# Kernel optimization log

Hardware: AMD Instinct MI355X
Metric: run time of the kernel (lower is better)

## Reference

```python
import jax, jax.numpy as jnp
import numpy as np

N, A, C = 2048, 256, 100   # batch, feat_dim, num_classes
LAT = A // 2               # latent_dim = feat_dim // 2
BN_EPS = 1e-5


def setup_inputs() -> dict:
    key = jax.random.key(0)
    ks = jax.random.split(key, 8)
    s = jax.random.normal(ks[0], (N, A), dtype=jnp.float32)
    y = jax.random.randint(ks[1], (N,), 0, C)
    ratio = jnp.float32(0.5)
    W1 = jax.random.normal(ks[2], (LAT, A), dtype=jnp.float32) / np.sqrt(A)
    b1 = jnp.zeros((LAT,), jnp.float32)
    gamma = jnp.ones((LAT,), jnp.float32)
    beta = jnp.zeros((LAT,), jnp.float32)
    W2 = jax.random.normal(ks[3], (A, LAT), dtype=jnp.float32) / np.sqrt(LAT)
    b2 = jnp.zeros((A,), jnp.float32)
    Wfc = jax.random.normal(ks[4], (C, A), dtype=jnp.float32) / np.sqrt(A)
    bfc = jnp.zeros((C,), jnp.float32)
    # per-class covariance table [C, A, A], symmetric PSD like a real EstimatorCV state
    M = jax.random.normal(ks[5], (C, A, A), dtype=jnp.float32)
    cov = jnp.einsum('cab,cdb->cad', M, M) / A
    return {"s": s, "y": y, "ratio": ratio, "W1": W1, "b1": b1,
            "gamma": gamma, "beta": beta, "W2": W2, "b2": b2,
            "Wfc": Wfc, "bfc": bfc, "cov": cov}


def reference(s, y, ratio, W1, b1, gamma, beta, W2, b2, Wfc, bfc, cov):
    # pred: Linear -> BatchNorm1d (train-mode batch stats) -> ReLU -> Linear -> ReLU
    h = s @ W1.T + b1                                   # [N, LAT]
    mu = jnp.mean(h, axis=0)
    var = jnp.var(h, axis=0)                            # biased, as torch BN
    h = (h - mu) / jnp.sqrt(var + BN_EPS) * gamma + beta
    h = jax.nn.relu(h)
    f = jax.nn.relu(h @ W2.T + b2)                      # [N, A]
    z = f @ Wfc.T + bfc                                 # [N, C]

    # correct_z: diag of (W_i - W_y) cov[y] (W_i - W_y)^T, computed without the
    # wasted off-diagonal bmm of the original
    cov_sg = jax.lax.stop_gradient(cov)                 # cov is detached in source
    Wy = Wfc[y]                                         # [N, A]
    diff = Wfc[None, :, :] - Wy[:, None, :]             # [N, C, A]
    CVy = cov_sg[y]                                     # [N, A, A]
    tmp = jnp.einsum('nca,nab->ncb', diff, CVy)         # [N, C, A]
    sigma2 = jnp.sum(tmp * diff, axis=-1)               # [N, C] = diag of quad form
    return z + ratio * 0.5 * sigma2
```

## Files before the change

kernel.cpp:

```cpp
#include <hip/hip_runtime.h>
#include <hip/hip_bf16.h>

#define Nn  2048
#define Aa  256
#define Cc  100
#define LAT 128
#define BN_EPS 1e-5f

#define OFF_HB   0
#define OFF_SUMS (OFF_HB + Nn*LAT/2)
#define OFF_SP   (OFF_SUMS + 128*256)
#define OFF_W2B  (OFF_SP + 4*Cc*Cc)
#define OFF_WFB  (OFF_W2B + Aa*LAT/2)

typedef __attribute__((ext_vector_type(8))) short bf16x8;
typedef __attribute__((ext_vector_type(4))) float f32x4;

__device__ __forceinline__ short f2bf(float f) {
    return (short)__bfloat16_as_ushort(__float2bfloat16(f));
}
__device__ __forceinline__ float bf2f(short h) {
    return __uint_as_float(((unsigned)(unsigned short)h) << 16);
}

#define DPITCH 264

__global__ __launch_bounds__(256) void kA(
    const float* __restrict__ s, const float* __restrict__ W1,
    const float* __restrict__ b1, const float* __restrict__ Wfc,
    const float* __restrict__ W2, const float* __restrict__ cov,
    short* __restrict__ hB, float* __restrict__ sums, float* __restrict__ Spart,
    short* __restrict__ W2b, short* __restrict__ Wfcb)
{
    __shared__ __align__(16) char smem[112 * DPITCH * 2 + 4 * 112 * 4];
    const int bid = blockIdx.x;
    const int t = threadIdx.x;
    const int w = t >> 6, l = t & 63, il = l & 15, q = l >> 4;

    if (bid < 400) {
        short* Dlds = (short*)smem;
        float (*red)[112] = (float(*)[112])(smem + 112 * DPITCH * 2);
        const int k  = bid >> 2;
        const int nq = bid & 3;
        const float* covk = cov + (size_t)k * (Aa * Aa);

        {
            const int c4 = t & 63;
            float4 wk = *(const float4*)&Wfc[(size_t)k * Aa + c4 * 4];
#pragma unroll
            for (int j = 0; j < 28; j++) {
                int row = (t >> 6) + j * 4;
                short4 o;
                if (row < Cc) {
                    float4 v = *(const float4*)&Wfc[(size_t)row * Aa + c4 * 4];
                    o.x = f2bf(v.x - wk.x); o.y = f2bf(v.y - wk.y);
                    o.z = f2bf(v.z - wk.z); o.w = f2bf(v.w - wk.w);
                } else {
                    o.x = 0; o.y = 0; o.z = 0; o.w = 0;
                }
                *(short4*)&Dlds[row * DPITCH + c4 * 4] = o;
            }
        }
        __syncthreads();

        const int bbase = nq * 64 + w * 16;

        f32x4 acc[7];
#pragma unroll
        for (int m = 0; m < 7; m++) acc[m] = (f32x4){0.f,0.f,0.f,0.f};

        const float* brow = covk + (size_t)(bbase + il) * Aa;

#pragma unroll
        for (int sgk = 0; sgk < 8; sgk++) {
            const int a0 = sgk * 32 + q * 8;
            float4 u0 = *(const float4*)&brow[a0];
            float4 u1 = *(const float4*)&brow[a0 + 4];
            bf16x8 bm;
            bm[0]=f2bf(u0.x); bm[1]=f2bf(u0.y); bm[2]=f2bf(u0.z); bm[3]=f2bf(u0.w);
            bm[4]=f2bf(u1.x); bm[5]=f2bf(u1.y); bm[6]=f2bf(u1.z); bm[7]=f2bf(u1.w);
#pragma unroll
            for (int m = 0; m < 7; m++) {
                bf16x8 am = *(bf16x8*)&Dlds[(m * 16 + il) * DPITCH + a0];
                acc[m] = __builtin_amdgcn_mfma_f32_16x16x32_bf16(am, bm, acc[m], 0, 0, 0);
            }
        }

#pragma unroll
        for (int m = 0; m < 7; m++) {
            const int bcol = bbase + il;
            float sacc[4];
#pragma unroll
            for (int r = 0; r < 4; r++) {
                int crow = m * 16 + q * 4 + r;
                sacc[r] = bf2f(Dlds[crow * DPITCH + bcol]) * acc[m][r];
            }
#pragma unroll
            for (int r = 0; r < 4; r++) {
                float v = sacc[r];
                v += __shfl_xor(v, 1);
                v += __shfl_xor(v, 2);
                v += __shfl_xor(v, 4);
                v += __shfl_xor(v, 8);
                if (il == 0) red[w][m * 16 + q * 4 + r] = v;
            }
        }
        __syncthreads();
        if (t < Cc)
            Spart[nq * (Cc * Cc) + k * Cc + t] =
                red[0][t] + red[1][t] + red[2][t] + red[3][t];
    } else if (bid < 528) {
        const int bid2 = bid - 400;
        const int row0 = bid2 * 16;
        const int colw = w * 32;

        f32x4 acc[2];
        acc[0] = (f32x4){0.f,0.f,0.f,0.f};
        acc[1] = (f32x4){0.f,0.f,0.f,0.f};

        const float* arow = s  + (size_t)(row0 + il) * Aa;
        const float* bp0  = W1 + (size_t)(colw + il) * Aa;
        const float* bp1  = W1 + (size_t)(colw + 16 + il) * Aa;

#pragma unroll
        for (int ks = 0; ks < 8; ks++) {
            const int k0 = ks * 32 + q * 8;
            float4 u0 = *(const float4*)&arow[k0];
            float4 u1 = *(const float4*)&arow[k0 + 4];
            bf16x8 am;
            am[0]=f2bf(u0.x); am[1]=f2bf(u0.y); am[2]=f2bf(u0.z); am[3]=f2bf(u0.w);
            am[4]=f2bf(u1.x); am[5]=f2bf(u1.y); am[6]=f2bf(u1.z); am[7]=f2bf(u1.w);
            float4 v0 = *(const float4*)&bp0[k0];
            float4 v1 = *(const float4*)&bp0[k0 + 4];
            bf16x8 bm0;
            bm0[0]=f2bf(v0.x); bm0[1]=f2bf(v0.y); bm0[2]=f2bf(v0.z); bm0[3]=f2bf(v0.w);
            bm0[4]=f2bf(v1.x); bm0[5]=f2bf(v1.y); bm0[6]=f2bf(v1.z); bm0[7]=f2bf(v1.w);
            float4 x0 = *(const float4*)&bp1[k0];
            float4 x1 = *(const float4*)&bp1[k0 + 4];
            bf16x8 bm1;
            bm1[0]=f2bf(x0.x); bm1[1]=f2bf(x0.y); bm1[2]=f2bf(x0.z); bm1[3]=f2bf(x0.w);
            bm1[4]=f2bf(x1.x); bm1[5]=f2bf(x1.y); bm1[6]=f2bf(x1.z); bm1[7]=f2bf(x1.w);
            acc[0] = __builtin_amdgcn_mfma_f32_16x16x32_bf16(am, bm0, acc[0], 0, 0, 0);
            acc[1] = __builtin_amdgcn_mfma_f32_16x16x32_bf16(am, bm1, acc[1], 0, 0, 0);
        }

#pragma unroll
        for (int n = 0; n < 2; n++) {
            const int col = colw + n * 16 + il;
            const float bias = b1[col];
            float s1 = 0.f, s2 = 0.f;
#pragma unroll
            for (int r = 0; r < 4; r++) {
                float v = acc[n][r] + bias;
                hB[(size_t)(row0 + q * 4 + r) * LAT + col] = f2bf(v);
                s1 += v; s2 += v * v;
            }
            s1 += __shfl_xor(s1, 16); s1 += __shfl_xor(s1, 32);
            s2 += __shfl_xor(s2, 16); s2 += __shfl_xor(s2, 32);
            if (q == 0) {
                sums[bid2 * 256 + col]       = s1;
                sums[bid2 * 256 + 128 + col] = s2;
            }
        }
    } else if (bid == 528) {
        for (int i = t * 4; i < Aa * LAT; i += 1024) {
            float4 v = *(const float4*)&W2[i];
            short4 o = {f2bf(v.x), f2bf(v.y), f2bf(v.z), f2bf(v.w)};
            *(short4*)&W2b[i] = o;
        }
    } else {
        for (int i = t * 4; i < 128 * Aa; i += 1024) {
            int row = i >> 8;
            short4 o = {0, 0, 0, 0};
            if (row < Cc) {
                float4 v = *(const float4*)&Wfc[i];
                o.x = f2bf(v.x); o.y = f2bf(v.y); o.z = f2bf(v.z); o.w = f2bf(v.w);
            }
            *(short4*)&Wfcb[i] = o;
        }
    }
}

#define FPITCH 264

__global__ __launch_bounds__(256) void kB(
    const short* __restrict__ hB, const float* __restrict__ sums,
    const float* __restrict__ gamma, const float* __restrict__ beta,
    const short* __restrict__ W2b, const float* __restrict__ b2,
    const short* __restrict__ Wfcb, const float* __restrict__ bfc,
    const float* __restrict__ Spart, const int* __restrict__ y,
    const float* __restrict__ ratio, float* __restrict__ out)
{
    __shared__ float scL[LAT], shL[LAT];
    __shared__ short fLDS[16 * FPITCH];
    const int t = threadIdx.x;
    const int w = t >> 6, l = t & 63, il = l & 15, q = l >> 4;
    const int row0 = blockIdx.x * 16;

    if (t < 128) {
        float a1 = 0.f, a2 = 0.f;
#pragma unroll 8
        for (int b = 0; b < 128; b++) {
            a1 += sums[b * 256 + t];
            a2 += sums[b * 256 + 128 + t];
        }
        float mu  = a1 * (1.0f / Nn);
        float var = a2 * (1.0f / Nn) - mu * mu;
        float inv = rsqrtf(var + BN_EPS);
        float sc  = gamma[t] * inv;
        scL[t] = sc;
        shL[t] = beta[t] - mu * sc;
    }
    __syncthreads();

    f32x4 acc3[4];
#pragma unroll
    for (int n = 0; n < 4; n++) acc3[n] = (f32x4){0.f,0.f,0.f,0.f};

    const short* arow = hB + (size_t)(row0 + il) * LAT;
#pragma unroll
    for (int ks = 0; ks < 4; ks++) {
        const int k0 = ks * 32 + q * 8;
        bf16x8 ha = *(const bf16x8*)&arow[k0];
        bf16x8 am;
#pragma unroll
        for (int j = 0; j < 8; j++) {
            float fv = fmaf(bf2f(ha[j]), scL[k0 + j], shL[k0 + j]);
            am[j] = f2bf(fmaxf(fv, 0.f));
        }
#pragma unroll
        for (int n = 0; n < 4; n++) {
            const int col = w * 64 + n * 16 + il;
            bf16x8 bm = *(const bf16x8*)&W2b[(size_t)col * LAT + k0];
            acc3[n] = __builtin_amdgcn_mfma_f32_16x16x32_bf16(am, bm, acc3[n], 0, 0, 0);
        }
    }
#pragma unroll
    for (int n = 0; n < 4; n++) {
        const int col = w * 64 + n * 16 + il;
        const float bias = b2[col];
#pragma unroll
        for (int r = 0; r < 4; r++) {
            float v = fmaxf(acc3[n][r] + bias, 0.f);
            fLDS[(q * 4 + r) * FPITCH + col] = f2bf(v);
        }
    }
    __syncthreads();

    f32x4 acc4[2];
    acc4[0] = (f32x4){0.f,0.f,0.f,0.f};
    acc4[1] = (f32x4){0.f,0.f,0.f,0.f};
#pragma unroll
    for (int ks = 0; ks < 8; ks++) {
        const int k0 = ks * 32 + q * 8;
        bf16x8 am = *(const bf16x8*)&fLDS[il * FPITCH + k0];
#pragma unroll
        for (int n = 0; n < 2; n++) {
            const int col = w * 32 + n * 16 + il;
            bf16x8 bm = *(const bf16x8*)&Wfcb[(size_t)col * Aa + k0];
            acc4[n] = __builtin_amdgcn_mfma_f32_16x16x32_bf16(am, bm, acc4[n], 0, 0, 0);
        }
    }

    const float coef = 0.5f * ratio[0];
    const int4 yv4 = *(const int4*)&y[row0 + q * 4];
    const int yr[4] = {yv4.x, yv4.y, yv4.z, yv4.w};

#pragma unroll
    for (int n = 0; n < 2; n++) {
        const int col = w * 32 + n * 16 + il;
        if (col < Cc) {
            const float bias = bfc[col];
#pragma unroll
            for (int r = 0; r < 4; r++) {
                const float* sp = &Spart[yr[r] * Cc + col];
                float sv = sp[0] + sp[Cc*Cc] + sp[2*Cc*Cc] + sp[3*Cc*Cc];
                out[(size_t)(row0 + q * 4 + r) * Cc + col] =
                    acc4[n][r] + bias + coef * sv;
            }
        }
    }
}

extern "C" void kernel_launch(void* const* d_in, const int* in_sizes, int n_in,
                              void* d_out, int out_size, void* d_ws, size_t ws_size,
                              hipStream_t stream)
{
    const float* s     = (const float*)d_in[0];
    const int*   y     = (const int*)  d_in[1];
    const float* ratio = (const float*)d_in[2];
    const float* W1    = (const float*)d_in[3];
    const float* b1    = (const float*)d_in[4];
    const float* gamma = (const float*)d_in[5];
    const float* beta  = (const float*)d_in[6];
    const float* W2    = (const float*)d_in[7];
    const float* b2    = (const float*)d_in[8];
    const float* Wfc   = (const float*)d_in[9];
    const float* bfc   = (const float*)d_in[10];
    const float* cov   = (const float*)d_in[11];
    float* out = (float*)d_out;
    float* ws  = (float*)d_ws;

    short* hB    = (short*)(ws + OFF_HB);
    float* sums  = ws + OFF_SUMS;
    float* Spart = ws + OFF_SP;
    short* W2b   = (short*)(ws + OFF_W2B);
    short* Wfcb  = (short*)(ws + OFF_WFB);

    hipLaunchKernelGGL(kA, dim3(530), dim3(256), 0, stream,
                       s, W1, b1, Wfc, W2, cov, hB, sums, Spart, W2b, Wfcb);
    hipLaunchKernelGGL(kB, dim3(128), dim3(256), 0, stream,
                       hB, sums, gamma, beta, W2b, b2, Wfcb, bfc, Spart, y, ratio, out);
}
```

Before: 35.24 us.

## Split sigma table blocks by class-row chunk and half of covariance columns

Each of the 400 sigma-table blocks previously covered all 112 padded class rows against a quarter of the covariance columns, so every block built the full Wfc-difference tile in LDS. Blocks now take a 64- or 48-row chunk of class rows against half of the covariance columns, with two column tiles per wave. This shrinks LDS use and the per-block diff-build work, and halves the number of partial sums the final kernel must add. In exchange each covariance row is read by two blocks instead of one, and the 48-row blocks do less work than the 64-row ones, so load is uneven.

Measured after the change: 34.80 us. About the same (-1.2%).

```diff
diff --git a/kernel.cpp b/kernel.cpp
--- a/kernel.cpp
+++ b/kernel.cpp
@@ -10,7 +10,7 @@
 #define OFF_HB   0
 #define OFF_SUMS (OFF_HB + Nn*LAT/2)
 #define OFF_SP   (OFF_SUMS + 128*256)
-#define OFF_W2B  (OFF_SP + 4*Cc*Cc)
+#define OFF_W2B  (OFF_SP + 2*Cc*Cc)
 #define OFF_WFB  (OFF_W2B + Aa*LAT/2)
 
 typedef __attribute__((ext_vector_type(8))) short bf16x8;
@@ -24,6 +24,99 @@
 }
 
 #define DPITCH 264
+
+template<int MSZ>
+__device__ __forceinline__ void ks_body(
+    const float* __restrict__ Wfc, const float* __restrict__ cov,
+    float* __restrict__ Spart, short* Dlds, float (*red)[64],
+    int k, int ch, int bh, int t, int w, int il, int q)
+{
+    const float* covk = cov + (size_t)k * (Aa * Aa);
+    const int c0 = ch * 64;
+
+    {
+        const int c4 = t & 63;
+        float4 wk = *(const float4*)&Wfc[(size_t)k * Aa + c4 * 4];
+#pragma unroll
+        for (int j = 0; j < MSZ * 4; j++) {
+            int row = (t >> 6) + j * 4;
+            int g = c0 + row;
+            short4 o = {0, 0, 0, 0};
+            if (g < Cc) {
+                float4 v = *(const float4*)&Wfc[(size_t)g * Aa + c4 * 4];
+                o.x = f2bf(v.x - wk.x); o.y = f2bf(v.y - wk.y);
+                o.z = f2bf(v.z - wk.z); o.w = f2bf(v.w - wk.w);
+            }
+            *(short4*)&Dlds[row * DPITCH + c4 * 4] = o;
+        }
+    }
+    __syncthreads();
+
+    const int bbase = bh * 128 + w * 32;
+
+    f32x4 acc[MSZ][2];
+#pragma unroll
+    for (int m = 0; m < MSZ; m++) {
+        acc[m][0] = (f32x4){0.f,0.f,0.f,0.f};
+        acc[m][1] = (f32x4){0.f,0.f,0.f,0.f};
+    }
+
+    const float* brow0 = covk + (size_t)(bbase + il) * Aa;
+    const float* brow1 = covk + (size_t)(bbase + 16 + il) * Aa;
+
+#pragma unroll
+    for (int sgk = 0; sgk < 8; sgk++) {
+        const int a0 = sgk * 32 + q * 8;
+        bf16x8 bm0, bm1;
+        {
+            float4 u0 = *(const float4*)&brow0[a0];
+            float4 u1 = *(const float4*)&brow0[a0 + 4];
+            bm0[0]=f2bf(u0.x); bm0[1]=f2bf(u0.y); bm0[2]=f2bf(u0.z); bm0[3]=f2bf(u0.w);
+            bm0[4]=f2bf(u1.x); bm0[5]=f2bf(u1.y); bm0[6]=f2bf(u1.z); bm0[7]=f2bf(u1.w);
+            float4 v0 = *(const float4*)&brow1[a0];
+            float4 v1 = *(const float4*)&brow1[a0 + 4];
+            bm1[0]=f2bf(v0.x); bm1[1]=f2bf(v0.y); bm1[2]=f2bf(v0.z); bm1[3]=f2bf(v0.w);
+            bm1[4]=f2bf(v1.x); bm1[5]=f2bf(v1.y); bm1[6]=f2bf(v1.z); bm1[7]=f2bf(v1.w);
+        }
+#pragma unroll
+        for (int m = 0; m < MSZ; m++) {
+            bf16x8 am = *(bf16x8*)&Dlds[(m * 16 + il) * DPITCH + a0];
+            acc[m][0] = __builtin_amdgcn_mfma_f32_16x16x32_bf16(am, bm0, acc[m][0], 0, 0, 0);
+            acc[m][1] = __builtin_amdgcn_mfma_f32_16x16x32_bf16(am, bm1, acc[m][1], 0, 0, 0);
+        }
+    }
+
+#pragma unroll
+    for (int m = 0; m < MSZ; m++) {
+        float sacc[4] = {0.f, 0.f, 0.f, 0.f};
+#pragma unroll
+        for (int nf = 0; nf < 2; nf++) {
+            int bcol = bbase + nf * 16 + il;
+#pragma unroll
+            for (int r = 0; r < 4; r++) {
+                int crow = m * 16 + q * 4 + r;
+                float dv = bf2f(Dlds[crow * DPITCH + bcol]);
+                sacc[r] = fmaf(dv, acc[m][nf][r], sacc[r]);
+            }
+        }
+#pragma unroll
+        for (int r = 0; r < 4; r++) {
+            float v = sacc[r];
+            v += __shfl_xor(v, 1);
+            v += __shfl_xor(v, 2);
+            v += __shfl_xor(v, 4);
+            v += __shfl_xor(v, 8);
+            if (il == 0) red[w][m * 16 + q * 4 + r] = v;
+        }
+    }
+    __syncthreads();
+    if (t < MSZ * 16) {
+        int c = c0 + t;
+        if (c < Cc)
+            Spart[bh * (Cc * Cc) + k * Cc + c] =
+                red[0][t] + red[1][t] + red[2][t] + red[3][t];
+    }
+}
 
 __global__ __launch_bounds__(256) void kA(
     const float* __restrict__ s, const float* __restrict__ W1,
@@ -32,83 +125,21 @@
     short* __restrict__ hB, float* __restrict__ sums, float* __restrict__ Spart,
     short* __restrict__ W2b, short* __restrict__ Wfcb)
 {
-    __shared__ __align__(16) char smem[112 * DPITCH * 2 + 4 * 112 * 4];
+    __shared__ __align__(16) char smem[64 * DPITCH * 2 + 4 * 64 * 4];
     const int bid = blockIdx.x;
     const int t = threadIdx.x;
     const int w = t >> 6, l = t & 63, il = l & 15, q = l >> 4;
 
     if (bid < 400) {
         short* Dlds = (short*)smem;
-        float (*red)[112] = (float(*)[112])(smem + 112 * DPITCH * 2);
+        float (*red)[64] = (float(*)[64])(smem + 64 * DPITCH * 2);
         const int k  = bid >> 2;
-        const int nq = bid & 3;
-        const float* covk = cov + (size_t)k * (Aa * Aa);
-
-        {
-            const int c4 = t & 63;
-            float4 wk = *(const float4*)&Wfc[(size_t)k * Aa + c4 * 4];
-#pragma unroll
-            for (int j = 0; j < 28; j++) {
-                int row = (t >> 6) + j * 4;
-                short4 o;
-                if (row < Cc) {
-                    float4 v = *(const float4*)&Wfc[(size_t)row * Aa + c4 * 4];
-                    o.x = f2bf(v.x - wk.x); o.y = f2bf(v.y - wk.y);
-                    o.z = f2bf(v.z - wk.z); o.w = f2bf(v.w - wk.w);
-                } else {
-                    o.x = 0; o.y = 0; o.z = 0; o.w = 0;
-                }
-                *(short4*)&Dlds[row * DPITCH + c4 * 4] = o;
-            }
-        }
-        __syncthreads();
-
-        const int bbase = nq * 64 + w * 16;
-
-        f32x4 acc[7];
-#pragma unroll
-        for (int m = 0; m < 7; m++) acc[m] = (f32x4){0.f,0.f,0.f,0.f};
-
-        const float* brow = covk + (size_t)(bbase + il) * Aa;
-
-#pragma unroll
-        for (int sgk = 0; sgk < 8; sgk++) {
-            const int a0 = sgk * 32 + q * 8;
-            float4 u0 = *(const float4*)&brow[a0];
-            float4 u1 = *(const float4*)&brow[a0 + 4];
-            bf16x8 bm;
-            bm[0]=f2bf(u0.x); bm[1]=f2bf(u0.y); bm[2]=f2bf(u0.z); bm[3]=f2bf(u0.w);
-            bm[4]=f2bf(u1.x); bm[5]=f2bf(u1.y); bm[6]=f2bf(u1.z); bm[7]=f2bf(u1.w);
-#pragma unroll
-            for (int m = 0; m < 7; m++) {
-                bf16x8 am = *(bf16x8*)&Dlds[(m * 16 + il) * DPITCH + a0];
-                acc[m] = __builtin_amdgcn_mfma_f32_16x16x32_bf16(am, bm, acc[m], 0, 0, 0);
-            }
-        }
-
-#pragma unroll
-        for (int m = 0; m < 7; m++) {
-            const int bcol = bbase + il;
-            float sacc[4];
-#pragma unroll
-            for (int r = 0; r < 4; r++) {
-                int crow = m * 16 + q * 4 + r;
-                sacc[r] = bf2f(Dlds[crow * DPITCH + bcol]) * acc[m][r];
-            }
-#pragma unroll
-            for (int r = 0; r < 4; r++) {
-                float v = sacc[r];
-                v += __shfl_xor(v, 1);
-                v += __shfl_xor(v, 2);
-                v += __shfl_xor(v, 4);
-                v += __shfl_xor(v, 8);
-                if (il == 0) red[w][m * 16 + q * 4 + r] = v;
-            }
-        }
-        __syncthreads();
-        if (t < Cc)
-            Spart[nq * (Cc * Cc) + k * Cc + t] =
-                red[0][t] + red[1][t] + red[2][t] + red[3][t];
+        const int ch = (bid >> 1) & 1;
+        const int bh = bid & 1;
+        if (ch == 0)
+            ks_body<4>(Wfc, cov, Spart, Dlds, red, k, 0, bh, t, w, il, q);
+        else
+            ks_body<3>(Wfc, cov, Spart, Dlds, red, k, 1, bh, t, w, il, q);
     } else if (bid < 528) {
         const int bid2 = bid - 400;
         const int row0 = bid2 * 16;
@@ -274,7 +305,7 @@
 #pragma unroll
             for (int r = 0; r < 4; r++) {
                 const float* sp = &Spart[yr[r] * Cc + col];
-                float sv = sp[0] + sp[Cc*Cc] + sp[2*Cc*Cc] + sp[3*Cc*Cc];
+                float sv = sp[0] + sp[Cc * Cc];
                 out[(size_t)(row0 + q * 4 + r) * Cc + col] =
                     acc4[n][r] + bias + coef * sv;
             }
```
